# Kernel tuning notes

Measured on AMD Instinct MI355X. Metric: run time of the kernel, lower is better.

Reference implementation:

```python
import jax, jax.numpy as jnp
import numpy as np
import math

INPUT_FRAMES = 12
FUTURE_FRAMES = 26
T_STEPS = INPUT_FRAMES + FUTURE_FRAMES - 1  # 37
HD = 64   # hidden_dim
D = 16    # d_attn
CIN = 3   # input channels (time='stable')
COUT = 2  # output_dim
H, W = 24, 48


def conv2d(x, w, b, pad):
    # x: (N,C,H,W), w: (O,I,kh,kw)
    y = jax.lax.conv_general_dilated(x, w, (1, 1), [(pad, pad), (pad, pad)],
                                     dimension_numbers=('NCHW', 'OIHW', 'NCHW'))
    return y + b[None, :, None, None]


def spatial_attn(q, k, v):
    # q,k,v: (N,C,S); attention over spatial dim S
    scale = 1.0 / math.sqrt(q.shape[1])
    scores = jnp.einsum('ncs,nct->nst', q, k) * scale  # (N,S,S)
    a = jax.nn.softmax(scores, axis=-1)
    return jnp.einsum('nst,nct->ncs', a, v)


def setup_inputs() -> dict:
    key = jax.random.key(0)
    ks = jax.random.split(key, 8)
    s = 0.05
    inp = {
        'input_x': jax.random.normal(ks[0], (16, T_STEPS, H, W, CIN), dtype=jnp.float32),
        # ConvLSTM gate conv: in = CIN+HD, out = 4*HD, 3x3
        'conv_w': jax.random.normal(ks[1], (4 * HD, CIN + HD, 3, 3), dtype=jnp.float32) * s,
        'conv_b': jnp.zeros((4 * HD,), jnp.float32),
        # SA memory module
        'h_w': jax.random.normal(ks[2], (3 * D, HD, 1, 1), dtype=jnp.float32) * s,
        'h_b': jnp.zeros((3 * D,), jnp.float32),
        'm_w': jax.random.normal(ks[3], (2 * D, HD, 1, 1), dtype=jnp.float32) * s,
        'm_b': jnp.zeros((2 * D,), jnp.float32),
        'z_w': jax.random.normal(ks[4], (D, 2 * D, 1, 1), dtype=jnp.float32) * s,
        'z_b': jnp.zeros((D,), jnp.float32),
        'o_w': jax.random.normal(ks[5], (3 * HD, HD + D, 3, 3), dtype=jnp.float32) * s,
        'o_b': jnp.zeros((3 * HD,), jnp.float32),
        # final 1x1 projection to output_dim
        'out_w': jax.random.normal(ks[6], (COUT, HD, 1, 1), dtype=jnp.float32) * s,
        'out_b': jnp.zeros((COUT,), jnp.float32),
    }
    return inp


def reference(input_x, conv_w, conv_b, h_w, h_b, m_w, m_b, z_w, z_b, o_w, o_b, out_w, out_b):
    x = jnp.transpose(input_x, (0, 1, 4, 2, 3))  # (N,T,C,H,W)
    N = x.shape[0]
    S = H * W

    h0 = jnp.zeros((N, HD, H, W), x.dtype)
    carry0 = (h0, h0, h0, jnp.zeros((N, COUT, H, W), x.dtype))

    def step(carry, inp_t):
        h, c, m, prev_out = carry
        xt, t = inp_t  # xt: (N,CIN,H,W), t: scalar
        autoreg = jnp.concatenate([prev_out, xt[:, 2:]], axis=1)
        feed = jnp.where(t < INPUT_FRAMES, xt, autoreg)
        # ConvLSTM gates
        comb = conv2d(jnp.concatenate([feed, h], axis=1), conv_w, conv_b, 1)
        ci, cf, co, cg = jnp.split(comb, 4, axis=1)
        i = jax.nn.sigmoid(ci)
        f = jax.nn.sigmoid(cf)
        o = jax.nn.sigmoid(co)
        g = jnp.tanh(cg)
        c = f * c + i * g
        h = o * jnp.tanh(c)
        # self-attention memory
        hq, hk, hv = jnp.split(conv2d(h, h_w, h_b, 0), 3, axis=1)
        mk, mv = jnp.split(conv2d(m, m_w, m_b, 0), 2, axis=1)
        Zh = spatial_attn(hq.reshape(N, D, S), hk.reshape(N, D, S), hv.reshape(N, D, S))
        Zm = spatial_attn(hq.reshape(N, D, S), mk.reshape(N, D, S), mv.reshape(N, D, S))
        Z = conv2d(jnp.concatenate([Zh.reshape(N, D, H, W), Zm.reshape(N, D, H, W)], axis=1), z_w, z_b, 0)
        iog = conv2d(jnp.concatenate([Z, h], axis=1), o_w, o_b, 1)
        si, sg, so = jnp.split(iog, 3, axis=1)
        si = jax.nn.sigmoid(si)
        sg = jnp.tanh(sg)
        m = si * sg + (1.0 - si) * m
        h = jax.nn.sigmoid(so) * m
        out = conv2d(h, out_w, out_b, 0)
        return (h, c, m, out), out

    xs = (jnp.transpose(x, (1, 0, 2, 3, 4)), jnp.arange(T_STEPS))
    _, outs = jax.lax.scan(step, carry0, xs)
    outputs = jnp.transpose(outs, (1, 0, 2, 3, 4))  # (N,T,COUT,H,W)

    nino = outputs[:, -FUTURE_FRAMES:, 0, 10:13, 19:30].mean(axis=(2, 3))  # (N,26)
    nino_pred = (nino[:, :-2] + nino[:, 1:-1] + nino[:, 2:]) / 3.0          # (N,24)
    return outputs, nino_pred
```

## Files before the change

kernel.cpp:

```cpp
#include <hip/hip_runtime.h>
#include <math.h>

#define HD 64
#define DATT 16
#define NCIN 3
#define NCOUT 2
#define HH 24
#define WW 48
#define SS (HH*WW)
#define NB 16
#define TSTEPS 37
#define INPUT_FRAMES 12

#define PR 26
#define PC 52
#define PHW (PR*PC)

#define OFF_H     0
#define OFF_C     1384448
#define OFF_M     2564096
#define OFF_FEED  3743744
#define OFF_Z     3808640
#define ZERO_END  4154752
#define OFF_QKV   4154752
#define OFF_MKV   5039488
#define OFF_HB    5629312
#define OFF_IOG   8873344
#define OFF_BF2   12412288
#define OFF_BF    12596864

typedef __attribute__((ext_vector_type(8))) short short8;
typedef __attribute__((ext_vector_type(4))) float f32x4;

__device__ __forceinline__ float sigmoidf_(float x) {
    return 1.0f / (1.0f + __expf(-x));
}
__device__ __forceinline__ unsigned short f2bf(float f) {
    unsigned u = __float_as_uint(f);
    unsigned r = (u + 0x7fffu + ((u >> 16) & 1u)) >> 16;
    return (unsigned short)r;
}
__device__ __forceinline__ float bf2f(unsigned short b) {
    return __uint_as_float(((unsigned)b) << 16);
}
__device__ __forceinline__ unsigned packbf(float f) {
    unsigned short hi = f2bf(f);
    unsigned short lo = f2bf(f - bf2f(hi));
    return ((unsigned)lo << 16) | (unsigned)hi;
}
__device__ __forceinline__ float unpackbf(unsigned pk) {
    return __uint_as_float(pk << 16) + __uint_as_float(pk & 0xffff0000u);
}
__device__ __forceinline__ unsigned cvt_pk_bf16(float a, float b) {
    unsigned r;
    asm("v_cvt_pk_bf16_f32 %0, %1, %2" : "=v"(r) : "v"(a), "v"(b));
    return r;
}
__device__ __forceinline__ int permrow(int t) {
    int kb = t >> 5, tl = t & 31;
    int quad = tl >> 3, rr = tl & 7;
    return kb * 32 + ((rr >= 4) ? 16 : 0) + quad * 4 + (rr & 3);
}

#define MKFRAG(P0, P1, ah, al) do {                                  \
    ah.i[0] = (P0.y << 16) | (P0.x & 0xffff);                        \
    ah.i[1] = (P0.w << 16) | (P0.z & 0xffff);                        \
    ah.i[2] = (P1.y << 16) | (P1.x & 0xffff);                        \
    ah.i[3] = (P1.w << 16) | (P1.z & 0xffff);                        \
    al.i[0] = (P0.y & 0xffff0000) | ((unsigned)P0.x >> 16);          \
    al.i[1] = (P0.w & 0xffff0000) | ((unsigned)P0.z >> 16);          \
    al.i[2] = (P1.y & 0xffff0000) | ((unsigned)P1.x >> 16);          \
    al.i[3] = (P1.w & 0xffff0000) | ((unsigned)P1.z >> 16);          \
} while (0)

__global__ void k_zero(float* __restrict__ p, int n4) {
    int i = blockIdx.x * blockDim.x + threadIdx.x;
    if (i < n4) ((float4*)p)[i] = make_float4(0.f, 0.f, 0.f, 0.f);
}

__global__ void k_prep_bf2(const float* __restrict__ cw, unsigned short* __restrict__ bbuf) {
    int idx = blockIdx.x * 256 + threadIdx.x;
    if (idx >= 344064) return;
    int j    = idx & 7;
    int lane = (idx >> 3) & 63;
    int ki   = (idx >> 9) % 21;
    int nt   = (idx / 10752) % 16;
    int p    = idx / 172032;
    int k = ki * 32 + (lane >> 4) * 8 + j;
    int ncol = nt * 16 + (lane & 15);
    unsigned short v = 0;
    if (k < 648) {
        int c = k % 72, kt = k / 72;
        if (c < 67) {
            float w = cw[ncol * 603 + c * 9 + kt];
            unsigned short hi = f2bf(w);
            v = (p == 0) ? hi : f2bf(w - bf2f(hi));
        }
    }
    bbuf[idx] = v;
}

__global__ void k_prep_bf(const float* __restrict__ ow, unsigned short* __restrict__ bbuf) {
    int idx = blockIdx.x * 256 + threadIdx.x;
    if (idx >= 282624) return;
    int j    = idx & 7;
    int lane = (idx >> 3) & 63;
    int ki   = (idx >> 9) % 23;
    int nt   = (idx / 11776) % 12;
    int p    = idx / 141312;
    int k = ki * 32 + (lane >> 4) * 8 + j;
    int ncol = nt * 16 + (lane & 15);
    unsigned short v = 0;
    if (k < 720) {
        int c = k % 80, kt = k / 80;
        float w = ow[ncol * 720 + c * 9 + kt];
        unsigned short hi = f2bf(w);
        v = (p == 0) ? hi : f2bf(w - bf2f(hi));
    }
    bbuf[idx] = v;
}

__global__ void k_feed0(const float* __restrict__ x, unsigned* __restrict__ feed) {
    int i = blockIdx.x * blockDim.x + threadIdx.x;
    if (i >= NB * 3 * SS) return;
    int s = i % SS;
    int ch = (i / SS) % 3;
    int n = i / (3 * SS);
    int y = s / WW, xx = s % WW;
    float v = x[(((size_t)(n * TSTEPS + 0) * HH + y) * WW + xx) * NCIN + ch];
    feed[((size_t)(n * 3 + ch) * PR + (y + 1)) * PC + (xx + 1)] = packbf(v);
}

#define ASTR2 76
#define ZOFF2 (3*52*ASTR2)
__global__ __launch_bounds__(256) void k_conv_lstm_mfma(
    const unsigned* __restrict__ feed, const unsigned* __restrict__ hin,
    const unsigned short* __restrict__ bbuf, const float* __restrict__ cb,
    float* __restrict__ c, unsigned* __restrict__ hout)
{
    __shared__ __align__(16) int lds[3 * 52 * ASTR2 + 8];
    const int y0 = blockIdx.x;
    const int nb = blockIdx.y;
    const int n  = blockIdx.z;
    const int tid = threadIdx.x;

    const unsigned* fbase = feed + (size_t)n * 3 * PHW;
    const unsigned* hbase = hin + (size_t)n * HD * PHW;
    for (int e = tid; e < 2808; e += 256) {
        int grp = e / 156;
        int r2  = e - grp * 156;
        int pr = r2 / 52, pc = r2 - pr * 52;
        int cc0 = grp * 4;
        int vv[4];
#pragma unroll
        for (int j = 0; j < 4; ++j) {
            int cc = cc0 + j;
            int t = 0;
            if (cc < 3)        t = (int)fbase[(size_t)cc * PHW + (y0 + pr) * PC + pc];
            else if (cc < 67)  t = (int)hbase[(size_t)(cc - 3) * PHW + (y0 + pr) * PC + pc];
            vv[j] = t;
        }
        int4 v; v.x = vv[0]; v.y = vv[1]; v.z = vv[2]; v.w = vv[3];
        *(int4*)&lds[r2 * ASTR2 + cc0] = v;
    }
    if (tid < 8) lds[ZOFF2 + tid] = 0;
    __syncthreads();

    const int wv = tid >> 6;
    const int lane = tid & 63;
    const int mcol = lane & 15;
    const int quad = lane >> 4;

    f32x4 acc[2][3];
#pragma unroll
    for (int jg = 0; jg < 2; ++jg)
#pragma unroll
        for (int xt = 0; xt < 3; ++xt) acc[jg][xt] = (f32x4){0.f, 0.f, 0.f, 0.f};

    const unsigned short* b0 = bbuf + ((size_t)(wv * 4 + nb * 2 + 0) * 21) * 512 + lane * 8;
    const unsigned short* b1 = bbuf + ((size_t)(wv * 4 + nb * 2 + 1) * 21) * 512 + lane * 8;

    short8 cb0h = *(const short8*)(b0);
    short8 cb0l = *(const short8*)(b0 + 172032);
    short8 cb1h = *(const short8*)(b1);
    short8 cb1l = *(const short8*)(b1 + 172032);

    for (int ki = 0; ki < 21; ++ki) {
        int kn = (ki < 20) ? (ki + 1) * 512 : 20 * 512;
        short8 nb0h = *(const short8*)(b0 + kn);
        short8 nb0l = *(const short8*)(b0 + kn + 172032);
        short8 nb1h = *(const short8*)(b1 + kn);
        short8 nb1l = *(const short8*)(b1 + kn + 172032);

        int k0 = ki * 32 + quad * 8;
        int ab, step;
        if (k0 < 648) {
            int kt = k0 / 72;
            int c0 = k0 - kt * 72;
            int dy = kt / 3, dx = kt - dy * 3;
            ab = (dy * 52 + mcol + dx) * ASTR2 + c0;
            step = 16 * ASTR2;
        } else {
            ab = ZOFF2; step = 0;
        }
        int4 A0 = *(const int4*)&lds[ab],            A1 = *(const int4*)&lds[ab + 4];
        int4 B0 = *(const int4*)&lds[ab + step],     B1 = *(const int4*)&lds[ab + step + 4];
        int4 C0 = *(const int4*)&lds[ab + 2 * step], C1 = *(const int4*)&lds[ab + 2 * step + 4];

        union { int i[4]; short8 v; } ah, al;
        MKFRAG(A0, A1, ah, al);
        acc[0][0] = __builtin_amdgcn_mfma_f32_16x16x32_bf16(ah.v, cb0h, acc[0][0], 0, 0, 0);
        acc[0][0] = __builtin_amdgcn_mfma_f32_16x16x32_bf16(ah.v, cb0l, acc[0][0], 0, 0, 0);
        acc[0][0] = __builtin_amdgcn_mfma_f32_16x16x32_bf16(al.v, cb0h, acc[0][0], 0, 0, 0);
        acc[1][0] = __builtin_amdgcn_mfma_f32_16x16x32_bf16(ah.v, cb1h, acc[1][0], 0, 0, 0);
        acc[1][0] = __builtin_amdgcn_mfma_f32_16x16x32_bf16(ah.v, cb1l, acc[1][0], 0, 0, 0);
        acc[1][0] = __builtin_amdgcn_mfma_f32_16x16x32_bf16(al.v, cb1h, acc[1][0], 0, 0, 0);
        MKFRAG(B0, B1, ah, al);
        acc[0][1] = __builtin_amdgcn_mfma_f32_16x16x32_bf16(ah.v, cb0h, acc[0][1], 0, 0, 0);
        acc[0][1] = __builtin_amdgcn_mfma_f32_16x16x32_bf16(ah.v, cb0l, acc[0][1], 0, 0, 0);
        acc[0][1] = __builtin_amdgcn_mfma_f32_16x16x32_bf16(al.v, cb0h, acc[0][1], 0, 0, 0);
        acc[1][1] = __builtin_amdgcn_mfma_f32_16x16x32_bf16(ah.v, cb1h, acc[1][1], 0, 0, 0);
        acc[1][1] = __builtin_amdgcn_mfma_f32_16x16x32_bf16(ah.v, cb1l, acc[1][1], 0, 0, 0);
        acc[1][1] = __builtin_amdgcn_mfma_f32_16x16x32_bf16(al.v, cb1h, acc[1][1], 0, 0, 0);
        MKFRAG(C0, C1, ah, al);
        acc[0][2] = __builtin_amdgcn_mfma_f32_16x16x32_bf16(ah.v, cb0h, acc[0][2], 0, 0, 0);
        acc[0][2] = __builtin_amdgcn_mfma_f32_16x16x32_bf16(ah.v, cb0l, acc[0][2], 0, 0, 0);
        acc[0][2] = __builtin_amdgcn_mfma_f32_16x16x32_bf16(al.v, cb0h, acc[0][2], 0, 0, 0);
        acc[1][2] = __builtin_amdgcn_mfma_f32_16x16x32_bf16(ah.v, cb1h, acc[1][2], 0, 0, 0);
        acc[1][2] = __builtin_amdgcn_mfma_f32_16x16x32_bf16(ah.v, cb1l, acc[1][2], 0, 0, 0);
        acc[1][2] = __builtin_amdgcn_mfma_f32_16x16x32_bf16(al.v, cb1h, acc[1][2], 0, 0, 0);

        cb0h = nb0h; cb0l = nb0l; cb1h = nb1h; cb1l = nb1l;
    }

    __syncthreads();
    float* exch = (float*)lds;
#pragma unroll
    for (int jg = 0; jg < 2; ++jg)
#pragma unroll
        for (int xt = 0; xt < 3; ++xt)
#pragma unroll
            for (int r = 0; r < 4; ++r)
                exch[((wv * 2 + jg) * 3 + xt) * 272 + (quad * 4 + r) * 17 + mcol] = acc[jg][xt][r];
    __syncthreads();

    const int ch32 = tid & 31;
    const int xg = tid >> 5;
    const int jg = ch32 >> 4, col = ch32 & 15;
    const int gch = nb * 32 + ch32;
    const float bi = cb[gch], bfv = cb[64 + gch], bo = cb[128 + gch], bg = cb[192 + gch];
    size_t cbase = ((size_t)(n * HD + gch) * HH + y0) * WW;
    unsigned* hp = hout + ((size_t)(n * HD + gch) * PR + y0 + 1) * PC + 1;
#pragma unroll
    for (int k = 0; k < 6; ++k) {
        int x = xg * 6 + k;
        int xt = x >> 4, row = x & 15;
        float iv = sigmoidf_(exch[((0 * 2 + jg) * 3 + xt) * 272 + row * 17 + col] + bi);
        float fv = sigmoidf_(exch[((1 * 2 + jg) * 3 + xt) * 272 + row * 17 + col] + bfv);
        float ov = sigmoidf_(exch[((2 * 2 + jg) * 3 + xt) * 272 + row * 17 + col] + bo);
        float gv = tanhf    (exch[((3 * 2 + jg) * 3 + xt) * 272 + row * 17 + col] + bg);
        float cold = c[cbase + x];
        float cn = fv * cold + iv * gv;
        float hn = ov * tanhf(cn);
        c[cbase + x] = cn;
        hp[x] = packbf(hn);
    }
}

#define ASTR (84)
#define ZOFF (3*52*ASTR)
__global__ __launch_bounds__(192) void k_conv_sa(
    const unsigned* __restrict__ Zin, const unsigned* __restrict__ hin,
    const unsigned short* __restrict__ bbuf, const float* __restrict__ ob,
    float* __restrict__ m, unsigned* __restrict__ hout)
{
    __shared__ __align__(16) int lds[3 * 52 * ASTR + 8];
    const int y0 = blockIdx.x;
    const int cbk = blockIdx.y;
    const int n  = blockIdx.z;
    const int tid = threadIdx.x;

    const unsigned* zbase = Zin + (size_t)n * DATT * PHW;
    const unsigned* hbase = hin + (size_t)n * HD * PHW;
    for (int e = tid; e < 3120; e += 192) {
        int grp = e / 156;
        int r2  = e - grp * 156;
        int pr = r2 / 52, pc = r2 - pr * 52;
        int cc0 = grp * 4;
        int vv[4];
#pragma unroll
        for (int j = 0; j < 4; ++j) {
            int cc = cc0 + j;
            const unsigned* src = (cc < 16) ? (zbase + (size_t)cc * PHW)
                                            : (hbase + (size_t)(cc - 16) * PHW);
            vv[j] = (int)src[(y0 + pr) * PC + pc];
        }
        int4 v; v.x = vv[0]; v.y = vv[1]; v.z = vv[2]; v.w = vv[3];
        *(int4*)&lds[r2 * ASTR + cc0] = v;
    }
    if (tid < 8) lds[ZOFF + tid] = 0;
    __syncthreads();

    const int wv = tid >> 6;
    const int lane = tid & 63;
    const int mcol = lane & 15;
    const int quad = lane >> 4;

    f32x4 acc[2][3];
#pragma unroll
    for (int j = 0; j < 2; ++j)
#pragma unroll
        for (int xt = 0; xt < 3; ++xt) acc[j][xt] = (f32x4){0.f, 0.f, 0.f, 0.f};

    const unsigned short* b0 = bbuf + ((size_t)(wv * 4 + cbk * 2 + 0) * 23) * 512 + lane * 8;
    const unsigned short* b1 = bbuf + ((size_t)(wv * 4 + cbk * 2 + 1) * 23) * 512 + lane * 8;

    short8 cb0h = *(const short8*)(b0);
    short8 cb0l = *(const short8*)(b0 + 141312);
    short8 cb1h = *(const short8*)(b1);
    short8 cb1l = *(const short8*)(b1 + 141312);

    for (int ki = 0; ki < 23; ++ki) {
        int kn = (ki < 22) ? (ki + 1) * 512 : 22 * 512;
        short8 nb0h = *(const short8*)(b0 + kn);
        short8 nb0l = *(const short8*)(b0 + kn + 141312);
        short8 nb1h = *(const short8*)(b1 + kn);
        short8 nb1l = *(const short8*)(b1 + kn + 141312);

        int k0 = ki * 32 + quad * 8;
        int ab, step;
        if (k0 < 720) {
            int kt = k0 / 80;
            int c0 = k0 - kt * 80;
            int dy = kt / 3, dx = kt - dy * 3;
            ab = (dy * 52 + mcol + dx) * ASTR + c0;
            step = 16 * ASTR;
        } else {
            ab = ZOFF; step = 0;
        }
        int4 A0 = *(const int4*)&lds[ab],            A1 = *(const int4*)&lds[ab + 4];
        int4 B0 = *(const int4*)&lds[ab + step],     B1 = *(const int4*)&lds[ab + step + 4];
        int4 C0 = *(const int4*)&lds[ab + 2 * step], C1 = *(const int4*)&lds[ab + 2 * step + 4];

        union { int i[4]; short8 v; } ah, al;
        MKFRAG(A0, A1, ah, al);
        acc[0][0] = __builtin_amdgcn_mfma_f32_16x16x32_bf16(ah.v, cb0h, acc[0][0], 0, 0, 0);
        acc[0][0] = __builtin_amdgcn_mfma_f32_16x16x32_bf16(ah.v, cb0l, acc[0][0], 0, 0, 0);
        acc[0][0] = __builtin_amdgcn_mfma_f32_16x16x32_bf16(al.v, cb0h, acc[0][0], 0, 0, 0);
        acc[1][0] = __builtin_amdgcn_mfma_f32_16x16x32_bf16(ah.v, cb1h, acc[1][0], 0, 0, 0);
        acc[1][0] = __builtin_amdgcn_mfma_f32_16x16x32_bf16(ah.v, cb1l, acc[1][0], 0, 0, 0);
        acc[1][0] = __builtin_amdgcn_mfma_f32_16x16x32_bf16(al.v, cb1h, acc[1][0], 0, 0, 0);
        MKFRAG(B0, B1, ah, al);
        acc[0][1] = __builtin_amdgcn_mfma_f32_16x16x32_bf16(ah.v, cb0h, acc[0][1], 0, 0, 0);
        acc[0][1] = __builtin_amdgcn_mfma_f32_16x16x32_bf16(ah.v, cb0l, acc[0][1], 0, 0, 0);
        acc[0][1] = __builtin_amdgcn_mfma_f32_16x16x32_bf16(al.v, cb0h, acc[0][1], 0, 0, 0);
        acc[1][1] = __builtin_amdgcn_mfma_f32_16x16x32_bf16(ah.v, cb1h, acc[1][1], 0, 0, 0);
        acc[1][1] = __builtin_amdgcn_mfma_f32_16x16x32_bf16(ah.v, cb1l, acc[1][1], 0, 0, 0);
        acc[1][1] = __builtin_amdgcn_mfma_f32_16x16x32_bf16(al.v, cb1h, acc[1][1], 0, 0, 0);
        MKFRAG(C0, C1, ah, al);
        acc[0][2] = __builtin_amdgcn_mfma_f32_16x16x32_bf16(ah.v, cb0h, acc[0][2], 0, 0, 0);
        acc[0][2] = __builtin_amdgcn_mfma_f32_16x16x32_bf16(ah.v, cb0l, acc[0][2], 0, 0, 0);
        acc[0][2] = __builtin_amdgcn_mfma_f32_16x16x32_bf16(al.v, cb0h, acc[0][2], 0, 0, 0);
        acc[1][2] = __builtin_amdgcn_mfma_f32_16x16x32_bf16(ah.v, cb1h, acc[1][2], 0, 0, 0);
        acc[1][2] = __builtin_amdgcn_mfma_f32_16x16x32_bf16(ah.v, cb1l, acc[1][2], 0, 0, 0);
        acc[1][2] = __builtin_amdgcn_mfma_f32_16x16x32_bf16(al.v, cb1h, acc[1][2], 0, 0, 0);

        cb0h = nb0h; cb0l = nb0l; cb1h = nb1h; cb1l = nb1l;
    }

    __syncthreads();
    float* exch = (float*)lds;
#pragma unroll
    for (int j = 0; j < 2; ++j)
#pragma unroll
        for (int xt = 0; xt < 3; ++xt)
#pragma unroll
            for (int r = 0; r < 4; ++r)
                exch[((wv * 2 + j) * 3 + xt) * 272 + (quad * 4 + r) * 17 + mcol] = acc[j][xt][r];
    __syncthreads();

    const int ch32 = tid & 31;
    const int xg = tid >> 5;
    const int jg = ch32 >> 4, col = ch32 & 15;
    const int gch = cbk * 32 + ch32;
    const float bsi = ob[gch], bsg = ob[64 + gch], bso = ob[128 + gch];
    float* mrow = m + ((size_t)(n * HD + gch) * HH + y0) * WW;
    unsigned* hp = hout + ((size_t)(n * HD + gch) * PR + y0 + 1) * PC + 1;
#pragma unroll
    for (int k = 0; k < 8; ++k) {
        int x = xg * 8 + k;
        int xt = x >> 4, row = x & 15;
        float si = sigmoidf_(exch[((0 * 2 + jg) * 3 + xt) * 272 + row * 17 + col] + bsi);
        float sg = tanhf    (exch[((1 * 2 + jg) * 3 + xt) * 272 + row * 17 + col] + bsg);
        float so =           exch[((2 * 2 + jg) * 3 + xt) * 272 + row * 17 + col] + bso;
        float mo = mrow[x];
        float mn = si * sg + (1.f - si) * mo;
        mrow[x] = mn;
        hp[x] = packbf(sigmoidf_(so) * mn);
    }
}

__global__ __launch_bounds__(256) void k_qkv(
    const unsigned* __restrict__ h, const float* __restrict__ m,
    const float* __restrict__ hw, const float* __restrict__ hb,
    const float* __restrict__ mw, const float* __restrict__ mb,
    unsigned short* __restrict__ pl) {
    __shared__ float lw[512];
    __shared__ float lb[8];
    const int g = blockIdx.y;
    const int tid = threadIdx.x;
    const float* wsrc = (g < 6) ? (hw + g * 512) : (mw + (g - 6) * 512);
    const float* bsrc = (g < 6) ? (hb + g * 8) : (mb + (g - 6) * 8);
    for (int i = tid; i < 512; i += 256) lw[i] = wsrc[i];
    if (tid < 8) lb[tid] = bsrc[tid];
    __syncthreads();

    int idx = blockIdx.x * 256 + tid;
    int s = idx % SS;
    int n = idx / SS;

    float reg[HD];
    if (g < 6) {
        int y = s / WW, x = s % WW;
        const unsigned* src = h + (size_t)n * HD * PHW + (y + 1) * PC + (x + 1);
#pragma unroll
        for (int ic = 0; ic < HD; ++ic) reg[ic] = unpackbf(src[ic * PHW]);
    } else {
        const float* src = m + (size_t)n * HD * SS + s;
#pragma unroll
        for (int ic = 0; ic < HD; ++ic) reg[ic] = src[ic * SS];
    }

    float out[8];
#pragma unroll
    for (int j = 0; j < 8; ++j) {
        const float* wr = &lw[j * HD];
        float a = lb[j];
#pragma unroll
        for (int ic = 0; ic < HD; ++ic) a += reg[ic] * wr[ic];
        out[j] = a;
    }

    unsigned short* bq  = pl;
    unsigned short* akh = pl + 294912;
    unsigned short* akm = pl + 589824;
    unsigned short* bvh = pl + 884736;
    unsigned short* bvm = pl + 1179648;
    const int c0 = (g & 1) * 8;

    if (g < 2) {
        unsigned w0 = (unsigned)f2bf(out[0]) | ((unsigned)f2bf(out[1]) << 16);
        unsigned w1 = (unsigned)f2bf(out[2]) | ((unsigned)f2bf(out[3]) << 16);
        unsigned w2 = (unsigned)f2bf(out[4]) | ((unsigned)f2bf(out[5]) << 16);
        unsigned w3 = (unsigned)f2bf(out[6]) | ((unsigned)f2bf(out[7]) << 16);
        *(uint4*)&bq[((size_t)n * SS + s) * 16 + c0] = make_uint4(w0, w1, w2, w3);
    } else if (g < 4 || (g >= 6 && g < 8)) {
        int row = permrow(s);
        unsigned short* base = (g < 4) ? akh : akm;
        unsigned w0 = (unsigned)f2bf(out[0]) | ((unsigned)f2bf(out[1]) << 16);
        unsigned w1 = (unsigned)f2bf(out[2]) | ((unsigned)f2bf(out[3]) << 16);
        unsigned w2 = (unsigned)f2bf(out[4]) | ((unsigned)f2bf(out[5]) << 16);
        unsigned w3 = (unsigned)f2bf(out[6]) | ((unsigned)f2bf(out[7]) << 16);
        *(uint4*)&base[((size_t)n * SS + row) * 16 + c0] = make_uint4(w0, w1, w2, w3);
    } else {
        unsigned short* base = (g < 6) ? bvh : bvm;
#pragma unroll
        for (int j = 0; j < 8; ++j)
            base[((size_t)n * 16 + c0 + j) * SS + s] = f2bf(out[j]);
    }
}

__global__ __launch_bounds__(256) void k_attn(
    const unsigned short* __restrict__ pl, const unsigned short* __restrict__ zbuf,
    const float* __restrict__ zw, const float* __restrict__ zb,
    unsigned* __restrict__ Z)
{
    __shared__ float ldsO[4][2][16][16];
    __shared__ float ldsF[2][16][16];
    __shared__ float ldsL[4][2][16];
    __shared__ float ldsLF[2][16];

    const int n   = blockIdx.x;
    const int qt  = blockIdx.y;
    const int tid = threadIdx.x;
    const int wv  = tid >> 6;
    const int lane = tid & 63;
    const int col  = lane & 15;
    const int quad = lane >> 4;
    const bool hi  = quad >= 2;

    const unsigned short* bq  = pl;
    const unsigned short* akh = pl + 294912;
    const unsigned short* akm = pl + 589824;
    const unsigned short* bvh = pl + 884736;
    const unsigned short* bvm = pl + 1179648;

    const size_t nb = (size_t)n * 18432;
    const int stepk = hi ? 0 : 512;
    const int subk  = hi ? 0 : 256;
    const unsigned short* qp  = hi ? zbuf : (bq  + nb + ((size_t)(qt * 16 + col)) * 16 + quad * 8);
    const unsigned short* khb = hi ? zbuf : (akh + nb + col * 16 + quad * 8);
    const unsigned short* kmb = hi ? zbuf : (akm + nb + col * 16 + quad * 8);
    const unsigned short* vhb = bvh + nb + (size_t)col * SS + quad * 8;
    const unsigned short* vmb = bvm + nb + (size_t)col * SS + quad * 8;

    short8 qf = *(const short8*)qp;

    f32x4 oh = (f32x4){0.f,0.f,0.f,0.f}, om = (f32x4){0.f,0.f,0.f,0.f};
    float lh = 0.f, lm = 0.f;
    const int kb0 = wv * 9, kb1 = kb0 + 9;
    for (int kb = kb0; kb < kb1; ++kb) {
        const unsigned short* kh0 = khb + (size_t)kb * stepk;
        const unsigned short* km0 = kmb + (size_t)kb * stepk;
        short8 khA = *(const short8*)kh0;
        short8 khB = *(const short8*)(kh0 + subk);
        short8 kmA = *(const short8*)km0;
        short8 kmB = *(const short8*)(km0 + subk);
        short8 vh  = *(const short8*)(vhb + (size_t)kb * 32);
        short8 vm  = *(const short8*)(vmb + (size_t)kb * 32);
        const f32x4 z4 = (f32x4){0.f,0.f,0.f,0.f};
        f32x4 sA = __builtin_amdgcn_mfma_f32_16x16x32_bf16(khA, qf, z4, 0, 0, 0);
        f32x4 sB = __builtin_amdgcn_mfma_f32_16x16x32_bf16(khB, qf, z4, 0, 0, 0);
        f32x4 tA = __builtin_amdgcn_mfma_f32_16x16x32_bf16(kmA, qf, z4, 0, 0, 0);
        f32x4 tB = __builtin_amdgcn_mfma_f32_16x16x32_bf16(kmB, qf, z4, 0, 0, 0);

        float pa0 = __expf(0.25f * sA[0]), pa1 = __expf(0.25f * sA[1]);
        float pa2 = __expf(0.25f * sA[2]), pa3 = __expf(0.25f * sA[3]);
        float pb0 = __expf(0.25f * sB[0]), pb1 = __expf(0.25f * sB[1]);
        float pb2 = __expf(0.25f * sB[2]), pb3 = __expf(0.25f * sB[3]);
        lh += (pa0 + pa1 + pa2 + pa3) + (pb0 + pb1 + pb2 + pb3);
        union { unsigned u[4]; short8 v; } ph;
        ph.u[0] = cvt_pk_bf16(pa0, pa1); ph.u[1] = cvt_pk_bf16(pa2, pa3);
        ph.u[2] = cvt_pk_bf16(pb0, pb1); ph.u[3] = cvt_pk_bf16(pb2, pb3);
        oh = __builtin_amdgcn_mfma_f32_16x16x32_bf16(ph.v, vh, oh, 0, 0, 0);

        float qa0 = __expf(0.25f * tA[0]), qa1 = __expf(0.25f * tA[1]);
        float qa2 = __expf(0.25f * tA[2]), qa3 = __expf(0.25f * tA[3]);
        float qb0 = __expf(0.25f * tB[0]), qb1 = __expf(0.25f * tB[1]);
        float qb2 = __expf(0.25f * tB[2]), qb3 = __expf(0.25f * tB[3]);
        lm += (qa0 + qa1 + qa2 + qa3) + (qb0 + qb1 + qb2 + qb3);
        union { unsigned u[4]; short8 v; } pm;
        pm.u[0] = cvt_pk_bf16(qa0, qa1); pm.u[1] = cvt_pk_bf16(qa2, qa3);
        pm.u[2] = cvt_pk_bf16(qb0, qb1); pm.u[3] = cvt_pk_bf16(qb2, qb3);
        om = __builtin_amdgcn_mfma_f32_16x16x32_bf16(pm.v, vm, om, 0, 0, 0);
    }

    lh += __shfl_xor(lh, 16); lh += __shfl_xor(lh, 32);
    lm += __shfl_xor(lm, 16); lm += __shfl_xor(lm, 32);

#pragma unroll
    for (int r = 0; r < 4; ++r) {
        ldsO[wv][0][quad * 4 + r][col] = oh[r];
        ldsO[wv][1][quad * 4 + r][col] = om[r];
    }
    if (lane < 16) { ldsL[wv][0][lane] = lh; ldsL[wv][1][lane] = lm; }
    __syncthreads();

    if (tid < 128) {
        int a_ = tid >> 6, rem = tid & 63, q_ = rem >> 2, j4 = (rem & 3) * 4;
        float4 s4 = make_float4(0.f, 0.f, 0.f, 0.f);
#pragma unroll
        for (int w = 0; w < 4; ++w) {
            float4 v = *(const float4*)&ldsO[w][a_][q_][j4];
            s4.x += v.x; s4.y += v.y; s4.z += v.z; s4.w += v.w;
        }
        *(float4*)&ldsF[a_][q_][j4] = s4;
    } else if (tid < 160) {
        int e = tid - 128, a_ = e >> 4, q_ = e & 15;
        ldsLF[a_][q_] = ldsL[0][a_][q_] + ldsL[1][a_][q_] +
                        ldsL[2][a_][q_] + ldsL[3][a_][q_];
    }
    __syncthreads();

    const int q  = tid & 15;
    const int zc = tid >> 4;
    float iLh = 1.f / ldsLF[0][q], iLm = 1.f / ldsLF[1][q];
    const float* zr = zw + zc * 32;
    float a = zb[zc];
#pragma unroll
    for (int j = 0; j < 16; ++j)
        a += zr[j] * (ldsF[0][q][j] * iLh) + zr[16 + j] * (ldsF[1][q][j] * iLm);
    int s = qt * 16 + q;
    int y = s / WW, x = s % WW;
    Z[((size_t)(n * DATT + zc) * PR + y + 1) * PC + x + 1] = packbf(a);
}

__global__ void k_out_feed(const unsigned* __restrict__ h, const float* __restrict__ ow,
                           const float* __restrict__ ob, const float* __restrict__ x,
                           float* __restrict__ outbuf, unsigned* __restrict__ feed, int t) {
    int idx = blockIdx.x * 256 + threadIdx.x;
    if (idx >= NB * SS) return;
    int s = idx % SS;
    int n = idx / SS;
    int y = s / WW, xx = s % WW;
    const unsigned* src = h + (size_t)n * HD * PHW + (y + 1) * PC + (xx + 1);
    float o0 = ob[0], o1 = ob[1];
#pragma unroll
    for (int ic = 0; ic < HD; ++ic) {
        float r = unpackbf(src[ic * PHW]);
        o0 += r * ow[ic];
        o1 += r * ow[HD + ic];
    }
    outbuf[(((size_t)n * TSTEPS + t) * NCOUT + 0) * SS + s] = o0;
    outbuf[(((size_t)n * TSTEPS + t) * NCOUT + 1) * SS + s] = o1;

    if (t + 1 < TSTEPS) {
        int t1 = t + 1;
        const float* xp = &x[(((size_t)(n * TSTEPS + t1) * HH + y) * WW + xx) * NCIN];
        float f0, f1, f2 = xp[2];
        if (t1 < INPUT_FRAMES) { f0 = xp[0]; f1 = xp[1]; }
        else { f0 = o0; f1 = o1; }
        size_t fb = ((size_t)(n * 3 + 0) * PR + y + 1) * PC + xx + 1;
        feed[fb] = packbf(f0);
        feed[fb + PHW] = packbf(f1);
        feed[fb + 2 * (size_t)PHW] = packbf(f2);
    }
}

__global__ void k_nino(const float* __restrict__ outbuf, float* __restrict__ pred) {
    int tidx = threadIdx.x;
    if (tidx >= 16 * 24) return;
    int j = tidx % 24;
    int n = tidx / 24;
    float acc = 0.f;
    for (int f = j; f < j + 3; ++f) {
        int t = 11 + f;
        const float* p = &outbuf[(((size_t)n * TSTEPS + t) * NCOUT + 0) * SS];
        float sloc = 0.f;
        for (int y = 10; y <= 12; ++y)
            for (int x = 19; x <= 29; ++x)
                sloc += p[y * WW + x];
        acc += sloc * (1.f / 33.f);
    }
    pred[n * 24 + j] = acc * (1.f / 3.f);
}

extern "C" void kernel_launch(void* const* d_in, const int* in_sizes, int n_in,
                              void* d_out, int out_size, void* d_ws, size_t ws_size,
                              hipStream_t stream) {
    const float* x      = (const float*)d_in[0];
    const float* conv_w = (const float*)d_in[1];
    const float* conv_b = (const float*)d_in[2];
    const float* h_w    = (const float*)d_in[3];
    const float* h_b    = (const float*)d_in[4];
    const float* m_w    = (const float*)d_in[5];
    const float* m_b    = (const float*)d_in[6];
    const float* z_w    = (const float*)d_in[7];
    const float* z_b    = (const float*)d_in[8];
    const float* o_w    = (const float*)d_in[9];
    const float* o_b    = (const float*)d_in[10];
    const float* out_w  = (const float*)d_in[11];
    const float* out_b  = (const float*)d_in[12];

    float* ws   = (float*)d_ws;
    unsigned* hA    = (unsigned*)(ws + OFF_H);
    float* c    = ws + OFF_C;
    float* m    = ws + OFF_M;
    unsigned* feedp = (unsigned*)(ws + OFF_FEED);
    unsigned* Zp    = (unsigned*)(ws + OFF_Z);
    unsigned* hB    = (unsigned*)(ws + OFF_HB);
    unsigned short* bf2 = (unsigned short*)(ws + OFF_BF2);
    unsigned short* bf  = (unsigned short*)(ws + OFF_BF);
    unsigned short* planes = (unsigned short*)(ws + OFF_QKV);
    const unsigned short* zbuf = (const unsigned short*)(ws + OFF_MKV);
    float* outp = (float*)d_out;

    k_zero<<<4058, 256, 0, stream>>>(ws, 1038688);
    k_zero<<<1352, 256, 0, stream>>>(ws + OFF_HB, 346112);
    k_zero<<<1, 64, 0, stream>>>(ws + OFF_MKV, 16);
    k_prep_bf2<<<1344, 256, 0, stream>>>(conv_w, bf2);
    k_prep_bf<<<1104, 256, 0, stream>>>(o_w, bf);
    k_feed0<<<216, 256, 0, stream>>>(x, feedp);

    for (int t = 0; t < TSTEPS; ++t) {
        k_conv_lstm_mfma<<<dim3(24, 2, 16), 256, 0, stream>>>(feedp, hB, bf2, conv_b, c, hA);
        k_qkv<<<dim3(72, 10), 256, 0, stream>>>(hA, m, h_w, h_b, m_w, m_b, planes);
        k_attn<<<dim3(16, 72), 256, 0, stream>>>(planes, zbuf, z_w, z_b, Zp);
        k_conv_sa<<<dim3(24, 2, 16), 192, 0, stream>>>(Zp, hA, bf, o_b, m, hB);
        k_out_feed<<<72, 256, 0, stream>>>(hB, out_w, out_b, x, outp, feedp, t);
    }
    k_nino<<<1, 384, 0, stream>>>(outp, outp + (size_t)NB * TSTEPS * NCOUT * SS);
}
```

Baseline: 3.915 ms.

## Pre-split bf16 hi/lo planes in LDS, deepen weight prefetch, reorder grid

Measured after the change: 4.205 ms. +7.4%, slower.

```diff
diff --git a/kernel.cpp b/kernel.cpp
--- a/kernel.cpp
+++ b/kernel.cpp
@@ -61,17 +61,6 @@
     int quad = tl >> 3, rr = tl & 7;
     return kb * 32 + ((rr >= 4) ? 16 : 0) + quad * 4 + (rr & 3);
 }
-
-#define MKFRAG(P0, P1, ah, al) do {                                  \
-    ah.i[0] = (P0.y << 16) | (P0.x & 0xffff);                        \
-    ah.i[1] = (P0.w << 16) | (P0.z & 0xffff);                        \
-    ah.i[2] = (P1.y << 16) | (P1.x & 0xffff);                        \
-    ah.i[3] = (P1.w << 16) | (P1.z & 0xffff);                        \
-    al.i[0] = (P0.y & 0xffff0000) | ((unsigned)P0.x >> 16);          \
-    al.i[1] = (P0.w & 0xffff0000) | ((unsigned)P0.z >> 16);          \
-    al.i[2] = (P1.y & 0xffff0000) | ((unsigned)P1.x >> 16);          \
-    al.i[3] = (P1.w & 0xffff0000) | ((unsigned)P1.z >> 16);          \
-} while (0)
 
 __global__ void k_zero(float* __restrict__ p, int n4) {
     int i = blockIdx.x * blockDim.x + threadIdx.x;
@@ -131,39 +120,46 @@
     feed[((size_t)(n * 3 + ch) * PR + (y + 1)) * PC + (xx + 1)] = packbf(v);
 }
 
-#define ASTR2 76
-#define ZOFF2 (3*52*ASTR2)
+#define RSTR2 304
+#define ZROW2 (156*RSTR2)
 __global__ __launch_bounds__(256) void k_conv_lstm_mfma(
     const unsigned* __restrict__ feed, const unsigned* __restrict__ hin,
     const unsigned short* __restrict__ bbuf, const float* __restrict__ cb,
     float* __restrict__ c, unsigned* __restrict__ hout)
 {
-    __shared__ __align__(16) int lds[3 * 52 * ASTR2 + 8];
-    const int y0 = blockIdx.x;
+    __shared__ __align__(16) int lds[156 * 76 + 76 + 8];
+    const int n  = blockIdx.x;
     const int nb = blockIdx.y;
-    const int n  = blockIdx.z;
+    const int y0 = blockIdx.z;
     const int tid = threadIdx.x;
 
     const unsigned* fbase = feed + (size_t)n * 3 * PHW;
     const unsigned* hbase = hin + (size_t)n * HD * PHW;
-    for (int e = tid; e < 2808; e += 256) {
+    for (int e = tid; e < 1404; e += 256) {
         int grp = e / 156;
         int r2  = e - grp * 156;
         int pr = r2 / 52, pc = r2 - pr * 52;
-        int cc0 = grp * 4;
-        int vv[4];
-#pragma unroll
-        for (int j = 0; j < 4; ++j) {
+        int cc0 = grp * 8;
+        unsigned v[8];
+#pragma unroll
+        for (int j = 0; j < 8; ++j) {
             int cc = cc0 + j;
-            int t = 0;
-            if (cc < 3)        t = (int)fbase[(size_t)cc * PHW + (y0 + pr) * PC + pc];
-            else if (cc < 67)  t = (int)hbase[(size_t)(cc - 3) * PHW + (y0 + pr) * PC + pc];
-            vv[j] = t;
-        }
-        int4 v; v.x = vv[0]; v.y = vv[1]; v.z = vv[2]; v.w = vv[3];
-        *(int4*)&lds[r2 * ASTR2 + cc0] = v;
-    }
-    if (tid < 8) lds[ZOFF2 + tid] = 0;
+            unsigned t = 0;
+            if (cc < 3)        t = fbase[(size_t)cc * PHW + (y0 + pr) * PC + pc];
+            else if (cc < 67)  t = hbase[(size_t)(cc - 3) * PHW + (y0 + pr) * PC + pc];
+            v[j] = t;
+        }
+        union { unsigned u[4]; short8 s; } hi8, lo8;
+#pragma unroll
+        for (int p = 0; p < 4; ++p) {
+            hi8.u[p] = (v[2 * p] & 0xffffu) | (v[2 * p + 1] << 16);
+            lo8.u[p] = (v[2 * p] >> 16) | (v[2 * p + 1] & 0xffff0000u);
+        }
+        char* rowp = (char*)lds + r2 * RSTR2 + cc0 * 2;
+        *(short8*)rowp = hi8.s;
+        *(short8*)(rowp + 144) = lo8.s;
+    }
+    for (int i = tid; i < 76; i += 256) lds[156 * 76 + i] = 0;
     __syncthreads();
 
     const int wv = tid >> 6;
@@ -184,53 +180,59 @@
     short8 cb0l = *(const short8*)(b0 + 172032);
     short8 cb1h = *(const short8*)(b1);
     short8 cb1l = *(const short8*)(b1 + 172032);
+    short8 pb0h = *(const short8*)(b0 + 512);
+    short8 pb0l = *(const short8*)(b0 + 512 + 172032);
+    short8 pb1h = *(const short8*)(b1 + 512);
+    short8 pb1l = *(const short8*)(b1 + 512 + 172032);
+
+    const char* lp = (const char*)lds;
 
     for (int ki = 0; ki < 21; ++ki) {
-        int kn = (ki < 20) ? (ki + 1) * 512 : 20 * 512;
-        short8 nb0h = *(const short8*)(b0 + kn);
-        short8 nb0l = *(const short8*)(b0 + kn + 172032);
-        short8 nb1h = *(const short8*)(b1 + kn);
-        short8 nb1l = *(const short8*)(b1 + kn + 172032);
+        int kn = (ki + 2 <= 20) ? (ki + 2) * 512 : 20 * 512;
+        short8 qb0h = *(const short8*)(b0 + kn);
+        short8 qb0l = *(const short8*)(b0 + kn + 172032);
+        short8 qb1h = *(const short8*)(b1 + kn);
+        short8 qb1l = *(const short8*)(b1 + kn + 172032);
 
         int k0 = ki * 32 + quad * 8;
-        int ab, step;
+        int abyte, stepb;
         if (k0 < 648) {
             int kt = k0 / 72;
             int c0 = k0 - kt * 72;
             int dy = kt / 3, dx = kt - dy * 3;
-            ab = (dy * 52 + mcol + dx) * ASTR2 + c0;
-            step = 16 * ASTR2;
+            abyte = (dy * 52 + mcol + dx) * RSTR2 + c0 * 2;
+            stepb = 16 * RSTR2;
         } else {
-            ab = ZOFF2; step = 0;
-        }
-        int4 A0 = *(const int4*)&lds[ab],            A1 = *(const int4*)&lds[ab + 4];
-        int4 B0 = *(const int4*)&lds[ab + step],     B1 = *(const int4*)&lds[ab + step + 4];
-        int4 C0 = *(const int4*)&lds[ab + 2 * step], C1 = *(const int4*)&lds[ab + 2 * step + 4];
-
-        union { int i[4]; short8 v; } ah, al;
-        MKFRAG(A0, A1, ah, al);
-        acc[0][0] = __builtin_amdgcn_mfma_f32_16x16x32_bf16(ah.v, cb0h, acc[0][0], 0, 0, 0);
-        acc[0][0] = __builtin_amdgcn_mfma_f32_16x16x32_bf16(ah.v, cb0l, acc[0][0], 0, 0, 0);
-        acc[0][0] = __builtin_amdgcn_mfma_f32_16x16x32_bf16(al.v, cb0h, acc[0][0], 0, 0, 0);
-        acc[1][0] = __builtin_amdgcn_mfma_f32_16x16x32_bf16(ah.v, cb1h, acc[1][0], 0, 0, 0);
-        acc[1][0] = __builtin_amdgcn_mfma_f32_16x16x32_bf16(ah.v, cb1l, acc[1][0], 0, 0, 0);
-        acc[1][0] = __builtin_amdgcn_mfma_f32_16x16x32_bf16(al.v, cb1h, acc[1][0], 0, 0, 0);
-        MKFRAG(B0, B1, ah, al);
-        acc[0][1] = __builtin_amdgcn_mfma_f32_16x16x32_bf16(ah.v, cb0h, acc[0][1], 0, 0, 0);
-        acc[0][1] = __builtin_amdgcn_mfma_f32_16x16x32_bf16(ah.v, cb0l, acc[0][1], 0, 0, 0);
-        acc[0][1] = __builtin_amdgcn_mfma_f32_16x16x32_bf16(al.v, cb0h, acc[0][1], 0, 0, 0);
-        acc[1][1] = __builtin_amdgcn_mfma_f32_16x16x32_bf16(ah.v, cb1h, acc[1][1], 0, 0, 0);
-        acc[1][1] = __builtin_amdgcn_mfma_f32_16x16x32_bf16(ah.v, cb1l, acc[1][1], 0, 0, 0);
-        acc[1][1] = __builtin_amdgcn_mfma_f32_16x16x32_bf16(al.v, cb1h, acc[1][1], 0, 0, 0);
-        MKFRAG(C0, C1, ah, al);
-        acc[0][2] = __builtin_amdgcn_mfma_f32_16x16x32_bf16(ah.v, cb0h, acc[0][2], 0, 0, 0);
-        acc[0][2] = __builtin_amdgcn_mfma_f32_16x16x32_bf16(ah.v, cb0l, acc[0][2], 0, 0, 0);
-        acc[0][2] = __builtin_amdgcn_mfma_f32_16x16x32_bf16(al.v, cb0h, acc[0][2], 0, 0, 0);
-        acc[1][2] = __builtin_amdgcn_mfma_f32_16x16x32_bf16(ah.v, cb1h, acc[1][2], 0, 0, 0);
-        acc[1][2] = __builtin_amdgcn_mfma_f32_16x16x32_bf16(ah.v, cb1l, acc[1][2], 0, 0, 0);
-        acc[1][2] = __builtin_amdgcn_mfma_f32_16x16x32_bf16(al.v, cb1h, acc[1][2], 0, 0, 0);
-
-        cb0h = nb0h; cb0l = nb0l; cb1h = nb1h; cb1l = nb1l;
+            abyte = ZROW2; stepb = 0;
+        }
+        short8 xh0 = *(const short8*)(lp + abyte);
+        short8 xl0 = *(const short8*)(lp + abyte + 144);
+        short8 xh1 = *(const short8*)(lp + abyte + stepb);
+        short8 xl1 = *(const short8*)(lp + abyte + stepb + 144);
+        short8 xh2 = *(const short8*)(lp + abyte + 2 * stepb);
+        short8 xl2 = *(const short8*)(lp + abyte + 2 * stepb + 144);
+
+        acc[0][0] = __builtin_amdgcn_mfma_f32_16x16x32_bf16(xh0, cb0h, acc[0][0], 0, 0, 0);
+        acc[0][0] = __builtin_amdgcn_mfma_f32_16x16x32_bf16(xh0, cb0l, acc[0][0], 0, 0, 0);
+        acc[0][0] = __builtin_amdgcn_mfma_f32_16x16x32_bf16(xl0, cb0h, acc[0][0], 0, 0, 0);
+        acc[1][0] = __builtin_amdgcn_mfma_f32_16x16x32_bf16(xh0, cb1h, acc[1][0], 0, 0, 0);
+        acc[1][0] = __builtin_amdgcn_mfma_f32_16x16x32_bf16(xh0, cb1l, acc[1][0], 0, 0, 0);
+        acc[1][0] = __builtin_amdgcn_mfma_f32_16x16x32_bf16(xl0, cb1h, acc[1][0], 0, 0, 0);
+        acc[0][1] = __builtin_amdgcn_mfma_f32_16x16x32_bf16(xh1, cb0h, acc[0][1], 0, 0, 0);
+        acc[0][1] = __builtin_amdgcn_mfma_f32_16x16x32_bf16(xh1, cb0l, acc[0][1], 0, 0, 0);
+        acc[0][1] = __builtin_amdgcn_mfma_f32_16x16x32_bf16(xl1, cb0h, acc[0][1], 0, 0, 0);
+        acc[1][1] = __builtin_amdgcn_mfma_f32_16x16x32_bf16(xh1, cb1h, acc[1][1], 0, 0, 0);
+        acc[1][1] = __builtin_amdgcn_mfma_f32_16x16x32_bf16(xh1, cb1l, acc[1][1], 0, 0, 0);
+        acc[1][1] = __builtin_amdgcn_mfma_f32_16x16x32_bf16(xl1, cb1h, acc[1][1], 0, 0, 0);
+        acc[0][2] = __builtin_amdgcn_mfma_f32_16x16x32_bf16(xh2, cb0h, acc[0][2], 0, 0, 0);
+        acc[0][2] = __builtin_amdgcn_mfma_f32_16x16x32_bf16(xh2, cb0l, acc[0][2], 0, 0, 0);
+        acc[0][2] = __builtin_amdgcn_mfma_f32_16x16x32_bf16(xl2, cb0h, acc[0][2], 0, 0, 0);
+        acc[1][2] = __builtin_amdgcn_mfma_f32_16x16x32_bf16(xh2, cb1h, acc[1][2], 0, 0, 0);
+        acc[1][2] = __builtin_amdgcn_mfma_f32_16x16x32_bf16(xh2, cb1l, acc[1][2], 0, 0, 0);
+        acc[1][2] = __builtin_amdgcn_mfma_f32_16x16x32_bf16(xl2, cb1h, acc[1][2], 0, 0, 0);
+
+        cb0h = pb0h; cb0l = pb0l; cb1h = pb1h; cb1l = pb1l;
+        pb0h = qb0h; pb0l = qb0l; pb1h = qb1h; pb1l = qb1l;
     }
 
     __syncthreads();
@@ -267,38 +269,45 @@
     }
 }
 
-#define ASTR (84)
-#define ZOFF (3*52*ASTR)
+#define RSTR 328
+#define ZROW (156*RSTR)
 __global__ __launch_bounds__(192) void k_conv_sa(
     const unsigned* __restrict__ Zin, const unsigned* __restrict__ hin,
     const unsigned short* __restrict__ bbuf, const float* __restrict__ ob,
     float* __restrict__ m, unsigned* __restrict__ hout)
 {
-    __shared__ __align__(16) int lds[3 * 52 * ASTR + 8];
-    const int y0 = blockIdx.x;
+    __shared__ __align__(16) int lds[156 * 82 + 82 + 8];
+    const int n  = blockIdx.x;
     const int cbk = blockIdx.y;
-    const int n  = blockIdx.z;
+    const int y0 = blockIdx.z;
     const int tid = threadIdx.x;
 
     const unsigned* zbase = Zin + (size_t)n * DATT * PHW;
     const unsigned* hbase = hin + (size_t)n * HD * PHW;
-    for (int e = tid; e < 3120; e += 192) {
+    for (int e = tid; e < 1560; e += 192) {
         int grp = e / 156;
         int r2  = e - grp * 156;
         int pr = r2 / 52, pc = r2 - pr * 52;
-        int cc0 = grp * 4;
-        int vv[4];
-#pragma unroll
-        for (int j = 0; j < 4; ++j) {
+        int cc0 = grp * 8;
+        unsigned v[8];
+#pragma unroll
+        for (int j = 0; j < 8; ++j) {
             int cc = cc0 + j;
             const unsigned* src = (cc < 16) ? (zbase + (size_t)cc * PHW)
                                             : (hbase + (size_t)(cc - 16) * PHW);
-            vv[j] = (int)src[(y0 + pr) * PC + pc];
-        }
-        int4 v; v.x = vv[0]; v.y = vv[1]; v.z = vv[2]; v.w = vv[3];
-        *(int4*)&lds[r2 * ASTR + cc0] = v;
-    }
-    if (tid < 8) lds[ZOFF + tid] = 0;
+            v[j] = src[(y0 + pr) * PC + pc];
+        }
+        union { unsigned u[4]; short8 s; } hi8, lo8;
+#pragma unroll
+        for (int p = 0; p < 4; ++p) {
+            hi8.u[p] = (v[2 * p] & 0xffffu) | (v[2 * p + 1] << 16);
+            lo8.u[p] = (v[2 * p] >> 16) | (v[2 * p + 1] & 0xffff0000u);
+        }
+        char* rowp = (char*)lds + r2 * RSTR + cc0 * 2;
+        *(short8*)rowp = hi8.s;
+        *(short8*)(rowp + 160) = lo8.s;
+    }
+    for (int i = tid; i < 82; i += 192) lds[156 * 82 + i] = 0;
     __syncthreads();
 
     const int wv = tid >> 6;
@@ -319,53 +328,59 @@
     short8 cb0l = *(const short8*)(b0 + 141312);
     short8 cb1h = *(const short8*)(b1);
     short8 cb1l = *(const short8*)(b1 + 141312);
+    short8 pb0h = *(const short8*)(b0 + 512);
+    short8 pb0l = *(const short8*)(b0 + 512 + 141312);
+    short8 pb1h = *(const short8*)(b1 + 512);
+    short8 pb1l = *(const short8*)(b1 + 512 + 141312);
+
+    const char* lp = (const char*)lds;
 
     for (int ki = 0; ki < 23; ++ki) {
-        int kn = (ki < 22) ? (ki + 1) * 512 : 22 * 512;
-        short8 nb0h = *(const short8*)(b0 + kn);
-        short8 nb0l = *(const short8*)(b0 + kn + 141312);
-        short8 nb1h = *(const short8*)(b1 + kn);
-        short8 nb1l = *(const short8*)(b1 + kn + 141312);
+        int kn = (ki + 2 <= 22) ? (ki + 2) * 512 : 22 * 512;
+        short8 qb0h = *(const short8*)(b0 + kn);
+        short8 qb0l = *(const short8*)(b0 + kn + 141312);
+        short8 qb1h = *(const short8*)(b1 + kn);
+        short8 qb1l = *(const short8*)(b1 + kn + 141312);
 
         int k0 = ki * 32 + quad * 8;
-        int ab, step;
+        int abyte, stepb;
         if (k0 < 720) {
             int kt = k0 / 80;
             int c0 = k0 - kt * 80;
             int dy = kt / 3, dx = kt - dy * 3;
-            ab = (dy * 52 + mcol + dx) * ASTR + c0;
-            step = 16 * ASTR;
+            abyte = (dy * 52 + mcol + dx) * RSTR + c0 * 2;
+            stepb = 16 * RSTR;
         } else {
-            ab = ZOFF; step = 0;
-        }
-        int4 A0 = *(const int4*)&lds[ab],            A1 = *(const int4*)&lds[ab + 4];
-        int4 B0 = *(const int4*)&lds[ab + step],     B1 = *(const int4*)&lds[ab + step + 4];
-        int4 C0 = *(const int4*)&lds[ab + 2 * step], C1 = *(const int4*)&lds[ab + 2 * step + 4];
-
-        union { int i[4]; short8 v; } ah, al;
-        MKFRAG(A0, A1, ah, al);
-        acc[0][0] = __builtin_amdgcn_mfma_f32_16x16x32_bf16(ah.v, cb0h, acc[0][0], 0, 0, 0);
-        acc[0][0] = __builtin_amdgcn_mfma_f32_16x16x32_bf16(ah.v, cb0l, acc[0][0], 0, 0, 0);
-        acc[0][0] = __builtin_amdgcn_mfma_f32_16x16x32_bf16(al.v, cb0h, acc[0][0], 0, 0, 0);
-        acc[1][0] = __builtin_amdgcn_mfma_f32_16x16x32_bf16(ah.v, cb1h, acc[1][0], 0, 0, 0);
-        acc[1][0] = __builtin_amdgcn_mfma_f32_16x16x32_bf16(ah.v, cb1l, acc[1][0], 0, 0, 0);
-        acc[1][0] = __builtin_amdgcn_mfma_f32_16x16x32_bf16(al.v, cb1h, acc[1][0], 0, 0, 0);
-        MKFRAG(B0, B1, ah, al);
-        acc[0][1] = __builtin_amdgcn_mfma_f32_16x16x32_bf16(ah.v, cb0h, acc[0][1], 0, 0, 0);
-        acc[0][1] = __builtin_amdgcn_mfma_f32_16x16x32_bf16(ah.v, cb0l, acc[0][1], 0, 0, 0);
-        acc[0][1] = __builtin_amdgcn_mfma_f32_16x16x32_bf16(al.v, cb0h, acc[0][1], 0, 0, 0);
-        acc[1][1] = __builtin_amdgcn_mfma_f32_16x16x32_bf16(ah.v, cb1h, acc[1][1], 0, 0, 0);
-        acc[1][1] = __builtin_amdgcn_mfma_f32_16x16x32_bf16(ah.v, cb1l, acc[1][1], 0, 0, 0);
-        acc[1][1] = __builtin_amdgcn_mfma_f32_16x16x32_bf16(al.v, cb1h, acc[1][1], 0, 0, 0);
-        MKFRAG(C0, C1, ah, al);
-        acc[0][2] = __builtin_amdgcn_mfma_f32_16x16x32_bf16(ah.v, cb0h, acc[0][2], 0, 0, 0);
-        acc[0][2] = __builtin_amdgcn_mfma_f32_16x16x32_bf16(ah.v, cb0l, acc[0][2], 0, 0, 0);
-        acc[0][2] = __builtin_amdgcn_mfma_f32_16x16x32_bf16(al.v, cb0h, acc[0][2], 0, 0, 0);
-        acc[1][2] = __builtin_amdgcn_mfma_f32_16x16x32_bf16(ah.v, cb1h, acc[1][2], 0, 0, 0);
-        acc[1][2] = __builtin_amdgcn_mfma_f32_16x16x32_bf16(ah.v, cb1l, acc[1][2], 0, 0, 0);
-        acc[1][2] = __builtin_amdgcn_mfma_f32_16x16x32_bf16(al.v, cb1h, acc[1][2], 0, 0, 0);
-
-        cb0h = nb0h; cb0l = nb0l; cb1h = nb1h; cb1l = nb1l;
+            abyte = ZROW; stepb = 0;
+        }
+        short8 xh0 = *(const short8*)(lp + abyte);
+        short8 xl0 = *(const short8*)(lp + abyte + 160);
+        short8 xh1 = *(const short8*)(lp + abyte + stepb);
+        short8 xl1 = *(const short8*)(lp + abyte + stepb + 160);
+        short8 xh2 = *(const short8*)(lp + abyte + 2 * stepb);
+        short8 xl2 = *(const short8*)(lp + abyte + 2 * stepb + 160);
+
+        acc[0][0] = __builtin_amdgcn_mfma_f32_16x16x32_bf16(xh0, cb0h, acc[0][0], 0, 0, 0);
+        acc[0][0] = __builtin_amdgcn_mfma_f32_16x16x32_bf16(xh0, cb0l, acc[0][0], 0, 0, 0);
+        acc[0][0] = __builtin_amdgcn_mfma_f32_16x16x32_bf16(xl0, cb0h, acc[0][0], 0, 0, 0);
+        acc[1][0] = __builtin_amdgcn_mfma_f32_16x16x32_bf16(xh0, cb1h, acc[1][0], 0, 0, 0);
+        acc[1][0] = __builtin_amdgcn_mfma_f32_16x16x32_bf16(xh0, cb1l, acc[1][0], 0, 0, 0);
+        acc[1][0] = __builtin_amdgcn_mfma_f32_16x16x32_bf16(xl0, cb1h, acc[1][0], 0, 0, 0);
+        acc[0][1] = __builtin_amdgcn_mfma_f32_16x16x32_bf16(xh1, cb0h, acc[0][1], 0, 0, 0);
+        acc[0][1] = __builtin_amdgcn_mfma_f32_16x16x32_bf16(xh1, cb0l, acc[0][1], 0, 0, 0);
+        acc[0][1] = __builtin_amdgcn_mfma_f32_16x16x32_bf16(xl1, cb0h, acc[0][1], 0, 0, 0);
+        acc[1][1] = __builtin_amdgcn_mfma_f32_16x16x32_bf16(xh1, cb1h, acc[1][1], 0, 0, 0);
+        acc[1][1] = __builtin_amdgcn_mfma_f32_16x16x32_bf16(xh1, cb1l, acc[1][1], 0, 0, 0);
+        acc[1][1] = __builtin_amdgcn_mfma_f32_16x16x32_bf16(xl1, cb1h, acc[1][1], 0, 0, 0);
+        acc[0][2] = __builtin_amdgcn_mfma_f32_16x16x32_bf16(xh2, cb0h, acc[0][2], 0, 0, 0);
+        acc[0][2] = __builtin_amdgcn_mfma_f32_16x16x32_bf16(xh2, cb0l, acc[0][2], 0, 0, 0);
+        acc[0][2] = __builtin_amdgcn_mfma_f32_16x16x32_bf16(xl2, cb0h, acc[0][2], 0, 0, 0);
+        acc[1][2] = __builtin_amdgcn_mfma_f32_16x16x32_bf16(xh2, cb1h, acc[1][2], 0, 0, 0);
+        acc[1][2] = __builtin_amdgcn_mfma_f32_16x16x32_bf16(xh2, cb1l, acc[1][2], 0, 0, 0);
+        acc[1][2] = __builtin_amdgcn_mfma_f32_16x16x32_bf16(xl2, cb1h, acc[1][2], 0, 0, 0);
+
+        cb0h = pb0h; cb0l = pb0l; cb1h = pb1h; cb1l = pb1l;
+        pb0h = qb0h; pb0l = qb0l; pb1h = qb1h; pb1l = qb1l;
     }
 
     __syncthreads();
@@ -673,10 +688,10 @@
     k_feed0<<<216, 256, 0, stream>>>(x, feedp);
 
     for (int t = 0; t < TSTEPS; ++t) {
-        k_conv_lstm_mfma<<<dim3(24, 2, 16), 256, 0, stream>>>(feedp, hB, bf2, conv_b, c, hA);
+        k_conv_lstm_mfma<<<dim3(16, 2, 24), 256, 0, stream>>>(feedp, hB, bf2, conv_b, c, hA);
         k_qkv<<<dim3(72, 10), 256, 0, stream>>>(hA, m, h_w, h_b, m_w, m_b, planes);
         k_attn<<<dim3(16, 72), 256, 0, stream>>>(planes, zbuf, z_w, z_b, Zp);
-        k_conv_sa<<<dim3(24, 2, 16), 192, 0, stream>>>(Zp, hA, bf, o_b, m, hB);
+        k_conv_sa<<<dim3(16, 2, 24), 192, 0, stream>>>(Zp, hA, bf, o_b, m, hB);
         k_out_feed<<<72, 256, 0, stream>>>(hB, out_w, out_b, x, outp, feedp, t);
     }
     k_nino<<<1, 384, 0, stream>>>(outp, outp + (size_t)NB * TSTEPS * NCOUT * SS);
```
